# Performance work log

Measured on AMD Instinct MI355X. Metric: run time of the kernel, lower is better.

## Reference

```python
import jax, jax.numpy as jnp
import numpy as np

N_NODES = 50000
N_EDGES = 800000
F_IN = 128
HID = 128
F_OUT = 2


def setup_inputs() -> dict:
    key = jax.random.key(0)
    ks = jax.random.split(key, 12)
    s = lambda d: 1.0 / np.sqrt(d)
    return {
        "x": jax.random.normal(ks[0], (N_NODES, F_IN), dtype=jnp.float32),
        "edge_index": jax.random.randint(ks[1], (2, N_EDGES), 0, N_NODES, dtype=jnp.int64),
        "W1_root": jax.random.normal(ks[2], (F_IN, HID), dtype=jnp.float32) * s(F_IN),
        "W1_nbr": jax.random.normal(ks[3], (F_IN, HID), dtype=jnp.float32) * s(F_IN),
        "b1": jnp.zeros((HID,), dtype=jnp.float32),
        "W2_root": jax.random.normal(ks[4], (HID, HID), dtype=jnp.float32) * s(HID),
        "W2_nbr": jax.random.normal(ks[5], (HID, HID), dtype=jnp.float32) * s(HID),
        "b2": jnp.zeros((HID,), dtype=jnp.float32),
        "Wa": jax.random.normal(ks[6], (HID, HID), dtype=jnp.float32) * s(HID),
        "a_src": jax.random.normal(ks[7], (HID,), dtype=jnp.float32) * s(HID),
        "a_dst": jax.random.normal(ks[8], (HID,), dtype=jnp.float32) * s(HID),
        "Wfc": jax.random.normal(ks[9], (HID, F_OUT), dtype=jnp.float32) * s(HID),
        "bfc": jnp.zeros((F_OUT,), dtype=jnp.float32),
    }


def reference(x, edge_index, W1_root, W1_nbr, b1, W2_root, W2_nbr, b2,
              Wa, a_src, a_dst, Wfc, bfc):
    src = edge_index[0]
    dst = edge_index[1]
    N = x.shape[0]

    def graph_conv(h, Wr, Wn, b):
        # sum-aggregate neighbor features, then two linear maps (PyG GraphConv)
        agg = jax.ops.segment_sum(h[src], dst, num_segments=N)  # [N, d]
        return h @ Wr + agg @ Wn + b

    h = jax.nn.relu(graph_conv(x, W1_root, W1_nbr, b1))
    h = jax.nn.relu(graph_conv(h, W2_root, W2_nbr, b2))

    # GAT-style attention: e_ij = LeakyReLU(a_src . Wh_j + a_dst . Wh_i)
    ht = h @ Wa                      # [N, HID]
    s_src = ht @ a_src               # [N]
    s_dst = ht @ a_dst               # [N]
    e = jax.nn.leaky_relu(s_src[src] + s_dst[dst], negative_slope=0.2)  # [E]

    # segment softmax over incoming edges of each destination node
    m = jax.ops.segment_max(e, dst, num_segments=N)          # [N]
    ee = jnp.exp(e - m[dst])                                  # [E]
    denom = jax.ops.segment_sum(ee, dst, num_segments=N)     # [N]
    alpha = ee / (denom[dst] + 1e-16)                         # [E]

    out = jax.ops.segment_sum(alpha[:, None] * ht[src], dst, num_segments=N)  # [N, HID]
    return out @ Wfc + bfc
```

## Files before the change

kernel.cpp:

```cpp
#include <hip/hip_runtime.h>
#include <cstddef>
#include <cstdint>


typedef __attribute__((ext_vector_type(8))) short short8;
typedef __attribute__((ext_vector_type(4))) float f32x4;

#define NBUK 128
#define BSH  9
#define CHUNK 1568

__device__ __forceinline__ ushort f2b(float f) {
  uint32_t u = __float_as_uint(f);
  u += 0x7fffu + ((u >> 16) & 1u);
  return (ushort)(u >> 16);
}
__device__ __forceinline__ float b2f(ushort h) {
  return __uint_as_float(((uint32_t)h) << 16);
}
__device__ __forceinline__ float blo(uint32_t u) { return __uint_as_float(u << 16); }
__device__ __forceinline__ float bhi(uint32_t u) { return __uint_as_float(u & 0xffff0000u); }

__device__ __forceinline__ void gload_lds16(const void* g, void* l) {
  __builtin_amdgcn_global_load_lds(
      (const __attribute__((address_space(1))) void*)g,
      (__attribute__((address_space(3))) void*)l, 16, 0, 0);
}

#define ACC8(A, V)                                     \
  { A[0] += blo(V.x); A[1] += bhi(V.x);                \
    A[2] += blo(V.y); A[3] += bhi(V.y);                \
    A[4] += blo(V.z); A[5] += bhi(V.z);                \
    A[6] += blo(V.w); A[7] += bhi(V.w); }

#define ACC8W(A, V, T)                                 \
  { A[0] += (T) * blo(V.x); A[1] += (T) * bhi(V.x);    \
    A[2] += (T) * blo(V.y); A[3] += (T) * bhi(V.y);    \
    A[4] += (T) * blo(V.z); A[5] += (T) * bhi(V.z);    \
    A[6] += (T) * blo(V.w); A[7] += (T) * bhi(V.w); }


__global__ __launch_bounds__(256) void split_kernel(
    const float* __restrict__ in, ushort* __restrict__ hi,
    ushort* __restrict__ lo, int n) {
  int i = (blockIdx.x * blockDim.x + threadIdx.x) * 8;
  if (i >= n) return;
  float4 v0 = *(const float4*)(in + i);
  float4 v1 = *(const float4*)(in + i + 4);
  float v[8] = {v0.x, v0.y, v0.z, v0.w, v1.x, v1.y, v1.z, v1.w};
  short8 h, l;
  #pragma unroll
  for (int b = 0; b < 8; ++b) {
    ushort hh = f2b(v[b]);
    h[b] = (short)hh;
    l[b] = (short)f2b(v[b] - b2f(hh));
  }
  *(short8*)(hi + i) = h;
  *(short8*)(lo + i) = l;
}


__global__ __launch_bounds__(256) void wsplit_kernel(
    const float* __restrict__ W0, const float* __restrict__ W1,
    const float* __restrict__ W2, const float* __restrict__ W3,
    const float* __restrict__ W4,
    ushort* __restrict__ WhT, ushort* __restrict__ WlT,
    int* __restrict__ bcnt) {
  __shared__ float tile[128][128];
  int m = blockIdx.x;
  const float* W = (m == 0) ? W0 : (m == 1) ? W1 : (m == 2) ? W2 : (m == 3) ? W3 : W4;
  int t = threadIdx.x;
  if (m == 0 && t < NBUK) bcnt[t] = 0;
  #pragma unroll
  for (int i = 0; i < 64; ++i) {
    int idx = i * 256 + t;
    tile[idx >> 7][idx & 127] = W[idx];
  }
  __syncthreads();
  int j = t >> 1, k0 = (t & 1) * 64;
  size_t obase = (size_t)m * 16384 + (size_t)j * 128 + k0;
  #pragma unroll
  for (int c = 0; c < 8; ++c) {
    short8 h, l;
    #pragma unroll
    for (int b = 0; b < 8; ++b) {
      float v = tile[k0 + c * 8 + b][j];
      ushort hh = f2b(v);
      h[b] = (short)hh;
      l[b] = (short)f2b(v - b2f(hh));
    }
    *(short8*)(WhT + obase + c * 8) = h;
    *(short8*)(WlT + obase + c * 8) = l;
  }
}


__global__ __launch_bounds__(256) void bhist_kernel(
    const int* __restrict__ ei, int E, int* __restrict__ bcnt) {
  __shared__ int lh[NBUK];
  int t = threadIdx.x;
  if (t < NBUK) lh[t] = 0;
  __syncthreads();
  int base = blockIdx.x * CHUNK;
  int lim = base + CHUNK; if (lim > E) lim = E;
  for (int i = base + t; i < lim; i += 256) atomicAdd(&lh[ei[E + i] >> BSH], 1);
  __syncthreads();
  if (t < NBUK && lh[t]) atomicAdd(&bcnt[t], lh[t]);
}

__global__ __launch_bounds__(256) void bscan_kernel(
    const int* __restrict__ bcnt, int* __restrict__ bbase,
    int* __restrict__ gtail) {
  __shared__ int sA[NBUK], sB[NBUK];
  int t = threadIdx.x;
  if (t < NBUK) sA[t] = bcnt[t];
  __syncthreads();
  int *s = sA, *d = sB;
  for (int st = 1; st < NBUK; st <<= 1) {
    if (t < NBUK) d[t] = s[t] + ((t >= st) ? s[t - st] : 0);
    __syncthreads();
    int* tmp = s; s = d; d = tmp;
  }
  if (t < NBUK) {
    int exc = (t == 0) ? 0 : s[t - 1];
    bbase[t] = exc;
    gtail[t] = exc;
  }
  if (t == 0) bbase[NBUK] = s[NBUK - 1];
}

__global__ __launch_bounds__(256) void bscatter_kernel(
    const int* __restrict__ ei, int E, int* __restrict__ gtail,
    uint* __restrict__ pair) {
  __shared__ int lh[NBUK], sB[NBUK], lofs[NBUK], lcur[NBUK], gbase[NBUK];
  __shared__ uint buf[CHUNK];
  int t = threadIdx.x;
  if (t < NBUK) lh[t] = 0;
  __syncthreads();
  int base = blockIdx.x * CHUNK;
  int lim = base + CHUNK; if (lim > E) lim = E;
  for (int i = base + t; i < lim; i += 256) atomicAdd(&lh[ei[E + i] >> BSH], 1);
  __syncthreads();
  int *s = lh, *d = sB;
  for (int st = 1; st < NBUK; st <<= 1) {
    if (t < NBUK) d[t] = s[t] + ((t >= st) ? s[t - st] : 0);
    __syncthreads();
    int* tmp = s; s = d; d = tmp;
  }
  if (t < NBUK) {
    lofs[t] = (t == 0) ? 0 : s[t - 1];
    lcur[t] = lofs[t];
  }
  __syncthreads();
  for (int i = base + t; i < lim; i += 256) {
    int srcv = ei[i], dstv = ei[E + i];
    int bk = dstv >> BSH;
    int p = atomicAdd(&lcur[bk], 1);
    buf[p] = ((uint)bk << 25) | ((uint)(dstv & ((1 << BSH) - 1)) << 16) | (uint)srcv;
  }
  __syncthreads();
  if (t < NBUK) {
    int c = s[t] - lofs[t];
    gbase[t] = c ? atomicAdd(&gtail[t], c) : 0;
  }
  __syncthreads();
  int n = lim - base;
  for (int i = t; i < n; i += 256) {
    uint pk = buf[i];
    int b = (int)(pk >> 25);
    pair[gbase[b] + (i - lofs[b])] = pk;
  }
}

__global__ __launch_bounds__(256) void csrbuild_kernel(
    const uint* __restrict__ pair, const int* __restrict__ bbase,
    int* __restrict__ ofs, int* __restrict__ csr, int N, int E) {
  __shared__ int hA[512], hB[512];
  int b = blockIdx.x, t = threadIdx.x;
  int base = bbase[b], cnt = bbase[b + 1] - base;
  int node0 = b << BSH;
  int nn = N - node0; if (nn > 512) nn = 512;
  hA[t] = 0; hA[t + 256] = 0;
  __syncthreads();
  for (int i = t; i < cnt; i += 256)
    atomicAdd(&hA[(pair[base + i] >> 16) & 511], 1);
  __syncthreads();
  int *s = hA, *d = hB;
  for (int st = 1; st < 512; st <<= 1) {
    #pragma unroll
    for (int k = 0; k < 2; ++k) {
      int i = t + k * 256;
      d[i] = s[i] + ((i >= st) ? s[i - st] : 0);
    }
    __syncthreads();
    int* tmp = s; s = d; d = tmp;
  }
  #pragma unroll
  for (int k = 0; k < 2; ++k) {
    int i = t + k * 256;
    if (i < nn) ofs[node0 + i] = base + (i == 0 ? 0 : s[i - 1]);
  }
  if (t == 0 && node0 + nn >= N) ofs[N] = E;
  #pragma unroll
  for (int k = 0; k < 2; ++k) {
    int i = t + k * 256;
    d[i] = (i == 0 ? 0 : s[i - 1]);
  }
  __syncthreads();
  for (int i = t; i < cnt; i += 256) {
    uint pk = pair[base + i];
    int p = atomicAdd(&d[(pk >> 16) & 511], 1);
    csr[base + p] = (int)(pk & 0xffffu);
  }
}


__global__ __launch_bounds__(256) void agg_kernel(
    const ushort* __restrict__ Xh, const int* __restrict__ csr,
    const int* __restrict__ ofs, ushort* __restrict__ Gh,
    ushort* __restrict__ Gl, int N) {
  int node = (blockIdx.x * blockDim.x + threadIdx.x) >> 6;
  int lane = threadIdx.x & 63;
  if (node >= N) return;
  int g = lane >> 4, q = lane & 15;
  int beg = ofs[node], end = ofs[node + 1];
  int deg = end - beg;
  float a[8] = {};
  for (int base = g; base < deg; base += 16) {
    int ib = base + 4, ic = base + 8, id = base + 12;
    int sa = csr[beg + base];
    int sb = csr[beg + ((ib < deg) ? ib : 0)];
    int sc = csr[beg + ((ic < deg) ? ic : 0)];
    int se = csr[beg + ((id < deg) ? id : 0)];
    uint4 va = *(const uint4*)(Xh + (size_t)sa * 128 + q * 8);
    uint4 vb = *(const uint4*)(Xh + (size_t)sb * 128 + q * 8);
    uint4 vc = *(const uint4*)(Xh + (size_t)sc * 128 + q * 8);
    uint4 vd = *(const uint4*)(Xh + (size_t)se * 128 + q * 8);
    ACC8(a, va);
    if (ib < deg) ACC8(a, vb);
    if (ic < deg) ACC8(a, vc);
    if (id < deg) ACC8(a, vd);
  }
  #pragma unroll
  for (int b = 0; b < 8; ++b) {
    a[b] += __shfl_xor(a[b], 16);
    a[b] += __shfl_xor(a[b], 32);
  }
  if (lane < 16) {
    short8 h, l;
    #pragma unroll
    for (int b = 0; b < 8; ++b) {
      ushort hh = f2b(a[b]);
      h[b] = (short)hh;
      l[b] = (short)f2b(a[b] - b2f(hh));
    }
    *(short8*)(Gh + (size_t)node * 128 + q * 8) = h;
    *(short8*)(Gl + (size_t)node * 128 + q * 8) = l;
  }
}


template <int S, bool RELU, bool BIAS, bool DOTS>
__global__ __launch_bounds__(512, 2) void mgemm_kernel(
    const ushort* __restrict__ A1h, const ushort* __restrict__ A1l,
    const ushort* __restrict__ A2h, const ushort* __restrict__ A2l,
    const ushort* __restrict__ WhT, const ushort* __restrict__ WlT,
    const float* __restrict__ bias,
    const float* __restrict__ asp, const float* __restrict__ adp,
    float* __restrict__ ssrc, float* __restrict__ sdst,
    ushort* __restrict__ Ch, ushort* __restrict__ Cl, int M) {
  __shared__ char lds[2 * S * 16384];
  __shared__ float pm[DOTS ? 8 * 128 : 1];
  int t = threadIdx.x;
  int l = t & 63;
  int w = t >> 6;
  int j = (w << 4) + (l & 15);
  int krow0 = (l >> 4) * 8;
  int rowBase = blockIdx.x * 64;

  const ushort* srcs[4] = {A1h, A1l, (S > 1) ? A2h : A1h, (S > 1) ? A2l : A1l};
  int ldsWaveBase0 = (t & ~63) * 16;
  #pragma unroll
  for (int q = 0; q < 2 * S; ++q) {
    const char* gsrc = (const char*)srcs[q];
    #pragma unroll
    for (int part = 0; part < 2; ++part) {
      int c = part * 512 + t;
      int r = c >> 4;
      int cb = (c & 15) << 4;
      int row = rowBase + r;
      if (row >= M) row = M - 1;
      int sb = cb ^ ((r & 7) << 4);
      gload_lds16(gsrc + (size_t)row * 256 + sb,
                  &lds[q * 16384 + part * 8192 + ldsWaveBase0]);
    }
  }

  short8 wh[S][4], wl[S][4];
  #pragma unroll
  for (int s = 0; s < S; ++s) {
    #pragma unroll
    for (int ks = 0; ks < 4; ++ks) {
      size_t wb = (size_t)s * 16384 + (size_t)j * 128 + ks * 32 + krow0;
      wh[s][ks] = *(const short8*)(WhT + wb);
      wl[s][ks] = *(const short8*)(WlT + wb);
    }
  }

  __syncthreads();

  f32x4 acc[4];
  #pragma unroll
  for (int i = 0; i < 4; ++i) acc[i] = (f32x4){0.f, 0.f, 0.f, 0.f};

  #pragma unroll
  for (int rf = 0; rf < 4; ++rf) {
    int r = rf * 16 + (l & 15);
    int sw = (r & 7) << 4;
    int rb = r * 256;
    #pragma unroll
    for (int s = 0; s < S; ++s) {
      #pragma unroll
      for (int ks = 0; ks < 4; ++ks) {
        int off = rb + ((ks * 64 + (l >> 4) * 16) ^ sw);
        short8 ah = *(const short8*)&lds[(s * 2 + 0) * 16384 + off];
        short8 al = *(const short8*)&lds[(s * 2 + 1) * 16384 + off];
        acc[rf] = __builtin_amdgcn_mfma_f32_16x16x32_bf16(al, wh[s][ks], acc[rf], 0, 0, 0);
        acc[rf] = __builtin_amdgcn_mfma_f32_16x16x32_bf16(ah, wl[s][ks], acc[rf], 0, 0, 0);
        acc[rf] = __builtin_amdgcn_mfma_f32_16x16x32_bf16(ah, wh[s][ks], acc[rf], 0, 0, 0);
      }
    }
  }

  float bj = BIAS ? bias[j] : 0.f;
  #pragma unroll
  for (int rf = 0; rf < 4; ++rf) {
    int rbase = rowBase + rf * 16 + (l >> 4) * 4;
    #pragma unroll
    for (int r = 0; r < 4; ++r) {
      int row = rbase + r;
      if (row < M) {
        float v = acc[rf][r];
        if (BIAS) v += bj;
        if (RELU) v = fmaxf(v, 0.f);
        ushort h = f2b(v);
        Ch[(size_t)row * 128 + j] = h;
        Cl[(size_t)row * 128 + j] = f2b(v - b2f(h));
      }
    }
  }

  if constexpr (DOTS) {
    float as_ = asp[j], ad_ = adp[j];
    #pragma unroll
    for (int rf = 0; rf < 4; ++rf) {
      #pragma unroll
      for (int r = 0; r < 4; ++r) {
        float v = acc[rf][r];
        float vs = v * as_, vd = v * ad_;
        #pragma unroll
        for (int d = 1; d < 16; d <<= 1) {
          vs += __shfl_xor(vs, d);
          vd += __shfl_xor(vd, d);
        }
        if ((l & 15) == 0) {
          int rl = rf * 16 + (l >> 4) * 4 + r;
          pm[w * 128 + rl * 2 + 0] = vs;
          pm[w * 128 + rl * 2 + 1] = vd;
        }
      }
    }
    __syncthreads();
    if (t < 64) {
      int row = rowBase + t;
      if (row < M) {
        float vs = 0.f, vd = 0.f;
        #pragma unroll
        for (int ww = 0; ww < 8; ++ww) {
          vs += pm[ww * 128 + t * 2 + 0];
          vd += pm[ww * 128 + t * 2 + 1];
        }
        ssrc[row] = vs;
        sdst[row] = vd;
      }
    }
  }
}


__global__ __launch_bounds__(256) void attn_kernel(
    const ushort* __restrict__ HTh, const int* __restrict__ csr,
    const int* __restrict__ ofs, const float* __restrict__ ssrc,
    const float* __restrict__ sdst, const float* __restrict__ Wfc,
    const float* __restrict__ bfc, float* __restrict__ out, int N) {
  int n = (blockIdx.x * blockDim.x + threadIdx.x) >> 6;
  int lane = threadIdx.x & 63;
  if (n >= N) return;
  int beg = ofs[n], end = ofs[n + 1];
  int deg = end - beg;
  float sd = sdst[n];
  int g = lane >> 4, q = lane & 15;
  float a[8] = {};
  float inv = 0.f;

  if (deg > 0 && deg <= 64) {
    int s_ = csr[beg + ((lane < deg) ? lane : 0)];
    float e = ssrc[s_] + sd;
    e = (e >= 0.f) ? e : 0.2f * e;
    float m = (lane < deg) ? e : -3.4e38f;
    #pragma unroll
    for (int d = 32; d > 0; d >>= 1) m = fmaxf(m, __shfl_xor(m, d));
    float t = (lane < deg) ? __expf(e - m) : 0.f;
    float ssum = t;
    #pragma unroll
    for (int d = 32; d > 0; d >>= 1) ssum += __shfl_xor(ssum, d);
    inv = 1.0f / (ssum + 1e-16f);

    int trips = (deg + 15) >> 4;
    for (int k = 0; k < trips; ++k) {
      int ia = k * 16 + g;
      int ib = ia + 4, ic = ia + 8, id = ia + 12;
      int sa = __shfl(s_, ia & 63);
      int sb = __shfl(s_, ib & 63);
      int sc = __shfl(s_, ic & 63);
      int se = __shfl(s_, id & 63);
      float ta0 = __shfl(t, ia & 63);
      float tb0 = __shfl(t, ib & 63);
      float tc0 = __shfl(t, ic & 63);
      float td0 = __shfl(t, id & 63);
      float ta = (ia < deg) ? ta0 : 0.f;
      float tb = (ib < deg) ? tb0 : 0.f;
      float tc = (ic < deg) ? tc0 : 0.f;
      float td = (id < deg) ? td0 : 0.f;
      uint4 va = *(const uint4*)(HTh + (size_t)sa * 128 + q * 8);
      uint4 vb = *(const uint4*)(HTh + (size_t)sb * 128 + q * 8);
      uint4 vc = *(const uint4*)(HTh + (size_t)sc * 128 + q * 8);
      uint4 vd = *(const uint4*)(HTh + (size_t)se * 128 + q * 8);
      ACC8W(a, va, ta);
      ACC8W(a, vb, tb);
      ACC8W(a, vc, tc);
      ACC8W(a, vd, td);
    }
  } else if (deg > 64) {
    float m = -3.4e38f;
    for (int i = lane; i < deg; i += 64) {
      float e = ssrc[csr[beg + i]] + sd;
      e = (e >= 0.f) ? e : 0.2f * e;
      m = fmaxf(m, e);
    }
    #pragma unroll
    for (int d = 32; d > 0; d >>= 1) m = fmaxf(m, __shfl_xor(m, d));
    float ssum = 0.f;
    for (int i = lane; i < deg; i += 64) {
      float e = ssrc[csr[beg + i]] + sd;
      e = (e >= 0.f) ? e : 0.2f * e;
      ssum += __expf(e - m);
    }
    #pragma unroll
    for (int d = 32; d > 0; d >>= 1) ssum += __shfl_xor(ssum, d);
    inv = 1.0f / (ssum + 1e-16f);
    for (int i = g; i < deg; i += 4) {
      int s = csr[beg + i];
      float e = ssrc[s] + sd;
      e = (e >= 0.f) ? e : 0.2f * e;
      float t = __expf(e - m);
      uint4 v = *(const uint4*)(HTh + (size_t)s * 128 + q * 8);
      ACC8W(a, v, t);
    }
  }

  #pragma unroll
  for (int b = 0; b < 8; ++b) {
    a[b] += __shfl_xor(a[b], 16);
    a[b] += __shfl_xor(a[b], 32);
    a[b] *= inv;
  }

  float4 wf0 = *(const float4*)(Wfc + q * 16);
  float4 wf1 = *(const float4*)(Wfc + q * 16 + 4);
  float4 wf2 = *(const float4*)(Wfc + q * 16 + 8);
  float4 wf3 = *(const float4*)(Wfc + q * 16 + 12);
  float o0 = a[0] * wf0.x + a[1] * wf0.z + a[2] * wf1.x + a[3] * wf1.z +
             a[4] * wf2.x + a[5] * wf2.z + a[6] * wf3.x + a[7] * wf3.z;
  float o1 = a[0] * wf0.y + a[1] * wf0.w + a[2] * wf1.y + a[3] * wf1.w +
             a[4] * wf2.y + a[5] * wf2.w + a[6] * wf3.y + a[7] * wf3.w;
  #pragma unroll
  for (int d = 1; d < 16; d <<= 1) {
    o0 += __shfl_xor(o0, d);
    o1 += __shfl_xor(o1, d);
  }
  if (lane == 0) {
    out[(size_t)n * 2 + 0] = o0 + bfc[0];
    out[(size_t)n * 2 + 1] = o1 + bfc[1];
  }
}


static inline size_t align_up(size_t x, size_t a) { return (x + a - 1) & ~(a - 1); }

extern "C" void kernel_launch(void* const* d_in, const int* in_sizes, int n_in,
                              void* d_out, int out_size, void* d_ws, size_t ws_size,
                              hipStream_t stream) {
  const float* x     = (const float*)d_in[0];
  const int*   ei    = (const int*)d_in[1];
  const float* W1r   = (const float*)d_in[2];
  const float* W1n   = (const float*)d_in[3];
  const float* b1    = (const float*)d_in[4];
  const float* W2r   = (const float*)d_in[5];
  const float* W2n   = (const float*)d_in[6];
  const float* b2    = (const float*)d_in[7];
  const float* Wa    = (const float*)d_in[8];
  const float* a_src = (const float*)d_in[9];
  const float* a_dst = (const float*)d_in[10];
  const float* Wfc   = (const float*)d_in[11];
  const float* bfc   = (const float*)d_in[12];

  const int N = in_sizes[0] / 128;
  const int E = in_sizes[1] / 2;

  char* ws = (char*)d_ws;
  size_t off = 0;
  auto take = [&](size_t bytes) {
    char* p = ws + off;
    off = align_up(off + bytes, 256);
    return p;
  };
  const size_t NB = (size_t)N * 128 * 2;
  int*    ofs   = (int*)take((size_t)(N + 1) * 4);
  int*    csr   = (int*)take((size_t)E * 4);
  int*    bcnt  = (int*)take(NBUK * 4);
  int*    bbase = (int*)take((NBUK + 1) * 4);
  int*    gtail = (int*)take(NBUK * 4);
  uint*   pair  = (uint*)take((size_t)E * 4);
  float*  ssrc  = (float*)take((size_t)N * 4);
  float*  sdst  = (float*)take((size_t)N * 4);
  ushort* whT   = (ushort*)take((size_t)5 * 16384 * 2);
  ushort* wlT   = (ushort*)take((size_t)5 * 16384 * 2);
  ushort* bA    = (ushort*)take(NB);
  ushort* bB    = (ushort*)take(NB);
  ushort* bC    = (ushort*)take(NB);
  ushort* bD    = (ushort*)take(NB);
  ushort* bE    = (ushort*)take(NB);
  ushort* bF    = (ushort*)take(NB);

  const int nodeBlocks = (N + 3) / 4;
  const int gemmBlocks = (N + 63) / 64;
  const int splitBlocks = (N * 128 / 8 + 255) / 256;
  const int chunkBlocks = (E + CHUNK - 1) / CHUNK;
  const int bukBlocks   = (N + 511) / 512;

  wsplit_kernel<<<5, 256, 0, stream>>>(W1r, W1n, W2r, W2n, Wa, whT, wlT, bcnt);
  split_kernel<<<splitBlocks, 256, 0, stream>>>(x, bA, bB, N * 128);
  bhist_kernel<<<chunkBlocks, 256, 0, stream>>>(ei, E, bcnt);
  bscan_kernel<<<1, 256, 0, stream>>>(bcnt, bbase, gtail);
  bscatter_kernel<<<chunkBlocks, 256, 0, stream>>>(ei, E, gtail, pair);
  csrbuild_kernel<<<bukBlocks, 256, 0, stream>>>(pair, bbase, ofs, csr, N, E);

  agg_kernel<<<nodeBlocks, 256, 0, stream>>>(bA, csr, ofs, bC, bD, N);
  mgemm_kernel<2, true, true, false><<<gemmBlocks, 512, 0, stream>>>(
      bA, bB, bC, bD, whT, wlT, b1, nullptr, nullptr, nullptr, nullptr,
      bE, bF, N);

  agg_kernel<<<nodeBlocks, 256, 0, stream>>>(bE, csr, ofs, bC, bD, N);
  mgemm_kernel<2, true, true, false><<<gemmBlocks, 512, 0, stream>>>(
      bE, bF, bC, bD, whT + 2 * 16384, wlT + 2 * 16384, b2, nullptr, nullptr,
      nullptr, nullptr, bA, bB, N);

  mgemm_kernel<1, false, false, true><<<gemmBlocks, 512, 0, stream>>>(
      bA, bB, nullptr, nullptr, whT + 4 * 16384, wlT + 4 * 16384, nullptr,
      a_src, a_dst, ssrc, sdst, bC, bD, N);

  attn_kernel<<<nodeBlocks, 256, 0, stream>>>(
      bC, csr, ofs, ssrc, sdst, Wfc, bfc, (float*)d_out, N);
}
```

Before: 252.4 us.

## Fuse neighbor aggregation into GraphConv GEMM via LDS staging

Replaces the separate agg_kernel plus two-source GEMM with one fused kernel per GraphConv layer. Each block gathers and sums neighbor rows for its 64 nodes directly into swizzled LDS as hi/lo bf16, then runs the MFMA GEMM over the root and aggregated operands. This removes the global write and re-read of the aggregated buffers and two kernel launches. It also drops the unused low-part store of the attention-projection output. The cost is that gather latency now sits inside the GEMM blocks, which have lower occupancy (512 threads, 64 KB LDS) than the old node-per-wave gather kernel.

```diff
diff --git a/kernel.cpp b/kernel.cpp
--- a/kernel.cpp
+++ b/kernel.cpp
@@ -215,52 +215,135 @@
 }
 
 
-__global__ __launch_bounds__(256) void agg_kernel(
-    const ushort* __restrict__ Xh, const int* __restrict__ csr,
-    const int* __restrict__ ofs, ushort* __restrict__ Gh,
-    ushort* __restrict__ Gl, int N) {
-  int node = (blockIdx.x * blockDim.x + threadIdx.x) >> 6;
-  int lane = threadIdx.x & 63;
-  if (node >= N) return;
-  int g = lane >> 4, q = lane & 15;
-  int beg = ofs[node], end = ofs[node + 1];
-  int deg = end - beg;
-  float a[8] = {};
-  for (int base = g; base < deg; base += 16) {
-    int ib = base + 4, ic = base + 8, id = base + 12;
-    int sa = csr[beg + base];
-    int sb = csr[beg + ((ib < deg) ? ib : 0)];
-    int sc = csr[beg + ((ic < deg) ? ic : 0)];
-    int se = csr[beg + ((id < deg) ? id : 0)];
-    uint4 va = *(const uint4*)(Xh + (size_t)sa * 128 + q * 8);
-    uint4 vb = *(const uint4*)(Xh + (size_t)sb * 128 + q * 8);
-    uint4 vc = *(const uint4*)(Xh + (size_t)sc * 128 + q * 8);
-    uint4 vd = *(const uint4*)(Xh + (size_t)se * 128 + q * 8);
-    ACC8(a, va);
-    if (ib < deg) ACC8(a, vb);
-    if (ic < deg) ACC8(a, vc);
-    if (id < deg) ACC8(a, vd);
-  }
-  #pragma unroll
-  for (int b = 0; b < 8; ++b) {
-    a[b] += __shfl_xor(a[b], 16);
-    a[b] += __shfl_xor(a[b], 32);
-  }
-  if (lane < 16) {
-    short8 h, l;
+__global__ __launch_bounds__(512, 2) void fgemm_kernel(
+    const ushort* __restrict__ A1h, const ushort* __restrict__ A1l,
+    const int* __restrict__ csr, const int* __restrict__ ofs,
+    const ushort* __restrict__ WhT, const ushort* __restrict__ WlT,
+    const float* __restrict__ bias,
+    ushort* __restrict__ Ch, ushort* __restrict__ Cl, int M) {
+  __shared__ char lds[4 * 16384];
+  int t = threadIdx.x;
+  int l = t & 63;
+  int w = t >> 6;
+  int j = (w << 4) + (l & 15);
+  int krow0 = (l >> 4) * 8;
+  int rowBase = blockIdx.x * 64;
+
+  const ushort* srcs[2] = {A1h, A1l};
+  int ldsWaveBase0 = (t & ~63) * 16;
+  #pragma unroll
+  for (int qq = 0; qq < 2; ++qq) {
+    const char* gsrc = (const char*)srcs[qq];
+    #pragma unroll
+    for (int part = 0; part < 2; ++part) {
+      int c = part * 512 + t;
+      int r = c >> 4;
+      int cb = (c & 15) << 4;
+      int row = rowBase + r;
+      if (row >= M) row = M - 1;
+      int sb = cb ^ ((r & 7) << 4);
+      gload_lds16(gsrc + (size_t)row * 256 + sb,
+                  &lds[qq * 16384 + part * 8192 + ldsWaveBase0]);
+    }
+  }
+
+  short8 wh[2][4], wl[2][4];
+  #pragma unroll
+  for (int s = 0; s < 2; ++s) {
+    #pragma unroll
+    for (int ks = 0; ks < 4; ++ks) {
+      size_t wb = (size_t)s * 16384 + (size_t)j * 128 + ks * 32 + krow0;
+      wh[s][ks] = *(const short8*)(WhT + wb);
+      wl[s][ks] = *(const short8*)(WlT + wb);
+    }
+  }
+
+  int g = l >> 4, q4 = l & 15;
+  for (int rr = 0; rr < 8; ++rr) {
+    int r = w * 8 + rr;
+    int row = rowBase + r;
+    if (row >= M) row = M - 1;
+    int beg = ofs[row], end = ofs[row + 1];
+    int deg = end - beg;
+    float a[8] = {};
+    for (int base = g; base < deg; base += 16) {
+      int ib = base + 4, ic = base + 8, id = base + 12;
+      int sa = csr[beg + base];
+      int sb = csr[beg + ((ib < deg) ? ib : 0)];
+      int sc = csr[beg + ((ic < deg) ? ic : 0)];
+      int se = csr[beg + ((id < deg) ? id : 0)];
+      uint4 va = *(const uint4*)(A1h + (size_t)sa * 128 + q4 * 8);
+      uint4 vb = *(const uint4*)(A1h + (size_t)sb * 128 + q4 * 8);
+      uint4 vc = *(const uint4*)(A1h + (size_t)sc * 128 + q4 * 8);
+      uint4 vd = *(const uint4*)(A1h + (size_t)se * 128 + q4 * 8);
+      ACC8(a, va);
+      if (ib < deg) ACC8(a, vb);
+      if (ic < deg) ACC8(a, vc);
+      if (id < deg) ACC8(a, vd);
+    }
     #pragma unroll
     for (int b = 0; b < 8; ++b) {
-      ushort hh = f2b(a[b]);
-      h[b] = (short)hh;
-      l[b] = (short)f2b(a[b] - b2f(hh));
-    }
-    *(short8*)(Gh + (size_t)node * 128 + q * 8) = h;
-    *(short8*)(Gl + (size_t)node * 128 + q * 8) = l;
-  }
-}
-
-
-template <int S, bool RELU, bool BIAS, bool DOTS>
+      a[b] += __shfl_xor(a[b], 16);
+      a[b] += __shfl_xor(a[b], 32);
+    }
+    if (l < 16) {
+      short8 h8, l8;
+      #pragma unroll
+      for (int b = 0; b < 8; ++b) {
+        ushort hh = f2b(a[b]);
+        h8[b] = (short)hh;
+        l8[b] = (short)f2b(a[b] - b2f(hh));
+      }
+      int off = r * 256 + ((q4 * 16) ^ ((r & 7) << 4));
+      *(short8*)&lds[2 * 16384 + off] = h8;
+      *(short8*)&lds[3 * 16384 + off] = l8;
+    }
+  }
+
+  __syncthreads();
+
+  f32x4 acc[4];
+  #pragma unroll
+  for (int i = 0; i < 4; ++i) acc[i] = (f32x4){0.f, 0.f, 0.f, 0.f};
+
+  #pragma unroll
+  for (int rf = 0; rf < 4; ++rf) {
+    int r = rf * 16 + (l & 15);
+    int sw = (r & 7) << 4;
+    int rb = r * 256;
+    #pragma unroll
+    for (int s = 0; s < 2; ++s) {
+      #pragma unroll
+      for (int ks = 0; ks < 4; ++ks) {
+        int off = rb + ((ks * 64 + (l >> 4) * 16) ^ sw);
+        short8 ah = *(const short8*)&lds[(s * 2 + 0) * 16384 + off];
+        short8 al = *(const short8*)&lds[(s * 2 + 1) * 16384 + off];
+        acc[rf] = __builtin_amdgcn_mfma_f32_16x16x32_bf16(al, wh[s][ks], acc[rf], 0, 0, 0);
+        acc[rf] = __builtin_amdgcn_mfma_f32_16x16x32_bf16(ah, wl[s][ks], acc[rf], 0, 0, 0);
+        acc[rf] = __builtin_amdgcn_mfma_f32_16x16x32_bf16(ah, wh[s][ks], acc[rf], 0, 0, 0);
+      }
+    }
+  }
+
+  float bj = bias[j];
+  #pragma unroll
+  for (int rf = 0; rf < 4; ++rf) {
+    int rbase = rowBase + rf * 16 + (l >> 4) * 4;
+    #pragma unroll
+    for (int r = 0; r < 4; ++r) {
+      int row = rbase + r;
+      if (row < M) {
+        float v = fmaxf(acc[rf][r] + bj, 0.f);
+        ushort h = f2b(v);
+        Ch[(size_t)row * 128 + j] = h;
+        Cl[(size_t)row * 128 + j] = f2b(v - b2f(h));
+      }
+    }
+  }
+}
+
+
+template <int S, bool RELU, bool BIAS, bool DOTS, bool STORELO>
 __global__ __launch_bounds__(512, 2) void mgemm_kernel(
     const ushort* __restrict__ A1h, const ushort* __restrict__ A1l,
     const ushort* __restrict__ A2h, const ushort* __restrict__ A2l,
@@ -345,7 +428,7 @@
         if (RELU) v = fmaxf(v, 0.f);
         ushort h = f2b(v);
         Ch[(size_t)row * 128 + j] = h;
-        Cl[(size_t)row * 128 + j] = f2b(v - b2f(h));
+        if (STORELO) Cl[(size_t)row * 128 + j] = f2b(v - b2f(h));
       }
     }
   }
@@ -539,7 +622,6 @@
   ushort* bA    = (ushort*)take(NB);
   ushort* bB    = (ushort*)take(NB);
   ushort* bC    = (ushort*)take(NB);
-  ushort* bD    = (ushort*)take(NB);
   ushort* bE    = (ushort*)take(NB);
   ushort* bF    = (ushort*)take(NB);
 
@@ -556,19 +638,15 @@
   bscatter_kernel<<<chunkBlocks, 256, 0, stream>>>(ei, E, gtail, pair);
   csrbuild_kernel<<<bukBlocks, 256, 0, stream>>>(pair, bbase, ofs, csr, N, E);
 
-  agg_kernel<<<nodeBlocks, 256, 0, stream>>>(bA, csr, ofs, bC, bD, N);
-  mgemm_kernel<2, true, true, false><<<gemmBlocks, 512, 0, stream>>>(
-      bA, bB, bC, bD, whT, wlT, b1, nullptr, nullptr, nullptr, nullptr,
-      bE, bF, N);
-
-  agg_kernel<<<nodeBlocks, 256, 0, stream>>>(bE, csr, ofs, bC, bD, N);
-  mgemm_kernel<2, true, true, false><<<gemmBlocks, 512, 0, stream>>>(
-      bE, bF, bC, bD, whT + 2 * 16384, wlT + 2 * 16384, b2, nullptr, nullptr,
-      nullptr, nullptr, bA, bB, N);
-
-  mgemm_kernel<1, false, false, true><<<gemmBlocks, 512, 0, stream>>>(
+  fgemm_kernel<<<gemmBlocks, 512, 0, stream>>>(
+      bA, bB, csr, ofs, whT, wlT, b1, bE, bF, N);
+
+  fgemm_kernel<<<gemmBlocks, 512, 0, stream>>>(
+      bE, bF, csr, ofs, whT + 2 * 16384, wlT + 2 * 16384, b2, bA, bB, N);
+
+  mgemm_kernel<1, false, false, true, false><<<gemmBlocks, 512, 0, stream>>>(
       bA, bB, nullptr, nullptr, whT + 4 * 16384, wlT + 4 * 16384, nullptr,
-      a_src, a_dst, ssrc, sdst, bC, bD, N);
+      a_src, a_dst, ssrc, sdst, bC, nullptr, N);
 
   attn_kernel<<<nodeBlocks, 256, 0, stream>>>(
       bC, csr, ofs, ssrc, sdst, Wfc, bfc, (float*)d_out, N);
```

Result: slower. 273.7 us (+8.4%).
